# Performance work log

Hardware: AMD Instinct MI355X
Metric: run time of the kernel (lower is better)

## Reference

```python
import jax, jax.numpy as jnp
import numpy as np

NUM_GROUPS = 32
EPS = 1e-5


def group_norm(x, w, b):
    # x: [B,C,H,W], 32 groups
    B, C, H, W = x.shape
    xg = x.reshape(B, NUM_GROUPS, C // NUM_GROUPS, H, W)
    mean = xg.mean(axis=(2, 3, 4), keepdims=True)
    var = xg.var(axis=(2, 3, 4), keepdims=True)
    xn = ((xg - mean) * jax.lax.rsqrt(var + EPS)).reshape(B, C, H, W)
    return xn * w[None, :, None, None] + b[None, :, None, None]


def conv1x1(x, w, b):
    # x: [B,C,H,W], w: [O,C], b: [O]
    return jnp.einsum('bchw,oc->bohw', x, w) + b[None, :, None, None]


def setup_inputs() -> dict:
    key = jax.random.key(0)
    ks = jax.random.split(key, 7)
    B, C, H, W = 16, 512, 32, 32
    x = jax.random.normal(ks[0], (B, C, H, W), dtype=jnp.float32)
    gn_w = jnp.ones((C,), dtype=jnp.float32)
    gn_b = jnp.zeros((C,), dtype=jnp.float32)
    s = 1.0 / np.sqrt(C)
    qkv_w = jax.random.normal(ks[1], (3 * C, C), dtype=jnp.float32) * s
    qkv_b = jnp.zeros((3 * C,), dtype=jnp.float32)
    proj_w = jax.random.normal(ks[2], (C, C), dtype=jnp.float32) * s
    proj_b = jnp.zeros((C,), dtype=jnp.float32)
    return {"x": x, "gn_w": gn_w, "gn_b": gn_b, "qkv_w": qkv_w,
            "qkv_b": qkv_b, "proj_w": proj_w, "proj_b": proj_b}


def reference(x, gn_w, gn_b, qkv_w, qkv_b, proj_w, proj_b):
    B, C, H, W = x.shape
    qkv = conv1x1(group_norm(x, gn_w, gn_b), qkv_w, qkv_b)
    q, k, v = jnp.split(qkv, 3, axis=1)
    scale = (C // 8) ** (-0.5)
    # attn: [B, h, w, H, W]
    attn = jnp.einsum('bchw,bcHW->bhwHW', q * scale, k)
    # NOTE: faithful to original torch code: softmax over the LAST axis only
    attn = jax.nn.softmax(attn, axis=-1)
    out = jnp.einsum('bhwHW,bcHW->bchw', attn, v)
    return x + conv1x1(out, proj_w, proj_b)
```

## Files before the change

kernel.cpp:

```cpp
#include <hip/hip_runtime.h>
#include <hip/hip_bf16.h>

#define B_    16
#define C_    512
#define S_    1024
#define NGRP  32
#define CPG   16

typedef __attribute__((ext_vector_type(8))) short  short8;
typedef __attribute__((ext_vector_type(4))) short  short4v;
typedef __attribute__((ext_vector_type(4))) float  floatx4;

__device__ __forceinline__ unsigned short f2bf(float f) {
    __hip_bfloat16 h = __float2bfloat16(f);
    unsigned short u;
    __builtin_memcpy(&u, &h, 2);
    return u;
}

__global__ __launch_bounds__(256)
void gn_fused_kernel(const float* __restrict__ x, const float* __restrict__ w,
                     const float* __restrict__ bias, __hip_bfloat16* __restrict__ xnT) {
    int bg = blockIdx.x;
    int b = bg >> 5, g = bg & 31;
    const float4* xp = (const float4*)(x + (size_t)bg * (CPG * S_));
    int tid = threadIdx.x;

    float4 vv[16];
    float s = 0.f, ss = 0.f;
#pragma unroll
    for (int r = 0; r < 16; ++r) {
        float4 v = xp[r * 256 + tid];
        vv[r] = v;
        s  += v.x + v.y + v.z + v.w;
        ss += v.x*v.x + v.y*v.y + v.z*v.z + v.w*v.w;
    }
    for (int off = 32; off > 0; off >>= 1) {
        s  += __shfl_down(s, off);
        ss += __shfl_down(ss, off);
    }
    __shared__ float red[2][4];
    __shared__ float msh[2];
    int wid = tid >> 6, lane = tid & 63;
    if (lane == 0) { red[0][wid] = s; red[1][wid] = ss; }
    __syncthreads();
    if (tid == 0) {
        float a = 0.f, c = 0.f;
        for (int i = 0; i < 4; ++i) { a += red[0][i]; c += red[1][i]; }
        float mean = a / (float)(CPG * S_);
        float var  = c / (float)(CPG * S_) - mean * mean;
        msh[0] = mean;
        msh[1] = rsqrtf(var + 1e-5f);
    }
    __syncthreads();
    float mean = msh[0], inv = msh[1];

    float sc[16], sh[16];
#pragma unroll
    for (int c = 0; c < 16; ++c) {
        float wc = w[g * 16 + c];
        sc[c] = inv * wc;
        sh[c] = bias[g * 16 + c] - mean * inv * wc;
    }

#pragma unroll
    for (int kk = 0; kk < 4; ++kk) {
        unsigned short outp[16];
#pragma unroll
        for (int c = 0; c < 16; ++c) {
            float v = (kk == 0) ? vv[c].x : (kk == 1) ? vv[c].y : (kk == 2) ? vv[c].z : vv[c].w;
            outp[c] = f2bf(v * sc[c] + sh[c]);
        }
        int srow = 4 * tid + kk;
        unsigned short* dst = (unsigned short*)xnT + ((size_t)(b * S_ + srow) * C_ + g * 16);
        *(short8*)dst       = *(short8*)outp;
        *(short8*)(dst + 8) = *(short8*)(outp + 8);
    }
}

__global__ __launch_bounds__(256)
void prep_kernel(const float* __restrict__ qkv_w, const float* __restrict__ proj_w,
                 const float* __restrict__ qkv_b,
                 unsigned short* __restrict__ bufX,
                 unsigned short* __restrict__ bufY,
                 float* __restrict__ bqWk, float* __restrict__ biasvp)
{
    int blk = blockIdx.x;
    int tid = threadIdx.x;
    if (blk < 192) {
        __shared__ float T[64][65];
        int mat = blk >> 6, tile = blk & 63;
        int r0 = (tile >> 3) * 64, c0 = (tile & 7) * 64;
        const float* src; unsigned short* dst;
        if (mat == 0)      { src = qkv_w + 512 * 512;  dst = bufX; }
        else if (mat == 1) { src = qkv_w;              dst = bufY; }
        else               { src = qkv_w + 1024 * 512; dst = bufY + 262144; }
#pragma unroll
        for (int rr = 0; rr < 4; ++rr) {
            int sr = rr * 16 + (tid >> 4);
            int sc = (tid & 15) * 4;
            float4 v = *(const float4*)(src + (size_t)(c0 + sr) * 512 + r0 + sc);
            T[sc][sr] = v.x; T[sc + 1][sr] = v.y; T[sc + 2][sr] = v.z; T[sc + 3][sr] = v.w;
        }
        __syncthreads();
#pragma unroll
        for (int rr = 0; rr < 4; ++rr) {
            int dr = rr * 16 + (tid >> 4);
            int dc = (tid & 15) * 4;
            short4v o;
            o[0] = (short)f2bf(T[dr][dc]);     o[1] = (short)f2bf(T[dr][dc + 1]);
            o[2] = (short)f2bf(T[dr][dc + 2]); o[3] = (short)f2bf(T[dr][dc + 3]);
            *(short4v*)(dst + (size_t)(r0 + dr) * 512 + c0 + dc) = o;
        }
    } else if (blk < 256) {
        unsigned short* wp = bufX + 262144;
#pragma unroll
        for (int t = 0; t < 4; ++t) {
            int i = (blk - 192) * 4096 + t * 1024 + tid * 4;
            float4 v = *(const float4*)(proj_w + i);
            short4v o;
            o[0] = (short)f2bf(v.x); o[1] = (short)f2bf(v.y);
            o[2] = (short)f2bf(v.z); o[3] = (short)f2bf(v.w);
            *(short4v*)(wp + i) = o;
        }
    } else if (blk < 264) {
        int sub = blk - 256;
        int j = (sub & 1) * 256 + tid;
        int o0 = (sub >> 1) * 128;
        float acc = 0.f;
#pragma unroll 8
        for (int oo = 0; oo < 128; ++oo) {
            int o = o0 + oo;
            acc += qkv_b[o] * qkv_w[(size_t)(512 + o) * 512 + j];
        }
        atomicAdd(&bqWk[j], acc);
    } else {
        int wv = tid >> 6, lane = tid & 63;
        int c = (blk - 264) * 4 + wv;
        float s = 0.f;
#pragma unroll
        for (int t = 0; t < 8; ++t)
            s += proj_w[(size_t)c * 512 + t * 64 + lane] * qkv_b[1024 + t * 64 + lane];
        for (int off = 32; off > 0; off >>= 1) s += __shfl_down(s, off);
        if (lane == 0) biasvp[c] = s;
    }
}

template<int BIAS_MODE, bool OUT_BF16, bool RESID, bool SWIZ, int KTOT>
__global__ __launch_bounds__(256)
void mfma_gemm(const unsigned short* __restrict__ A, const unsigned short* __restrict__ Bm,
               const float* __restrict__ bias, const float* __restrict__ resid,
               void* __restrict__ Yv,
               int lda, int ldb, int ldy,
               size_t sA, size_t sB, size_t sY, size_t sR, float alpha,
               int ntsh, int nxsh)
{
    __shared__ unsigned short As[2 * 128 * 32];
    __shared__ unsigned short Bs[2 * 128 * 32];
    int bx, by, bz;
    if (SWIZ) {
        int lin = blockIdx.x;
        int xcd = lin & 7, sup = lin >> 3;
        bz = xcd + ((sup >> ntsh) << 3);
        int tile = sup & ((1 << ntsh) - 1);
        bx = tile & ((1 << nxsh) - 1);
        by = tile >> nxsh;
    } else { bx = blockIdx.x; by = blockIdx.y; bz = blockIdx.z; }

    const unsigned short* Ab = A  + (size_t)bz * sA;
    const unsigned short* Bb = Bm + (size_t)bz * sB;
    const int tid = threadIdx.x, wave = tid >> 6, lane = tid & 63;
    const int m0 = by * 128, n0 = bx * 128;
    const int wr = wave >> 1, wc = wave & 1, lr = lane & 15, kq = lane >> 4;
    const int row0 = tid >> 2, kc0 = (tid & 3) << 3;

    floatx4 acc[4][4] = {};

    for (int k0 = 0; k0 < KTOT; k0 += 64) {
        __syncthreads();
#pragma unroll
        for (int kk = 0; kk < 2; ++kk) {
#pragma unroll
            for (int r = 0; r < 2; ++r) {
                const unsigned short* ga = Ab + (size_t)(m0 + r * 64 + row0) * lda + k0 + kk * 32 + kc0;
                __builtin_amdgcn_global_load_lds(
                    (const __attribute__((address_space(1))) void*)ga,
                    (__attribute__((address_space(3))) void*)(As + kk * 4096 + (r * 256 + wave * 64) * 8),
                    16, 0, 0);
                const unsigned short* gb = Bb + (size_t)(n0 + r * 64 + row0) * ldb + k0 + kk * 32 + kc0;
                __builtin_amdgcn_global_load_lds(
                    (const __attribute__((address_space(1))) void*)gb,
                    (__attribute__((address_space(3))) void*)(Bs + kk * 4096 + (r * 256 + wave * 64) * 8),
                    16, 0, 0);
            }
        }
        __syncthreads();

#pragma unroll
        for (int kk = 0; kk < 2; ++kk) {
            short8 af[4], bfr[4];
#pragma unroll
            for (int i = 0; i < 4; ++i)
                af[i] = *(const short8*)&As[kk * 4096 + (wr * 64 + i * 16 + lr) * 32 + kq * 8];
#pragma unroll
            for (int j = 0; j < 4; ++j)
                bfr[j] = *(const short8*)&Bs[kk * 4096 + (wc * 64 + j * 16 + lr) * 32 + kq * 8];
#pragma unroll
            for (int i = 0; i < 4; ++i)
#pragma unroll
                for (int j = 0; j < 4; ++j)
                    acc[i][j] = __builtin_amdgcn_mfma_f32_16x16x32_bf16(af[i], bfr[j], acc[i][j], 0, 0, 0);
        }
    }

    const size_t ybase = (size_t)bz * sY;
    const size_t rbase = (size_t)bz * sR;
#pragma unroll
    for (int i = 0; i < 4; ++i) {
#pragma unroll
        for (int r = 0; r < 4; ++r) {
            int m = m0 + wr * 64 + i * 16 + kq * 4 + r;
            float bm = (BIAS_MODE == 1) ? bias[m] : 0.f;
#pragma unroll
            for (int j = 0; j < 4; ++j) {
                int n = n0 + wc * 64 + j * 16 + lr;
                float vv = acc[i][j][r] * alpha + bm;
                if (BIAS_MODE == 2) vv += bias[n];
                if (RESID) vv += resid[rbase + (size_t)m * ldy + n];
                if (OUT_BF16)
                    ((__hip_bfloat16*)Yv)[ybase + (size_t)m * ldy + n] = __float2bfloat16(vv);
                else
                    ((float*)Yv)[ybase + (size_t)m * ldy + n] = vv;
            }
        }
    }
}

template<int BIAS_MODE, bool OUT_BF16, bool RESID, bool SWIZ, int KTOT>
__global__ __launch_bounds__(512)
void gemm8ph(const unsigned short* __restrict__ A, const unsigned short* __restrict__ Bm,
             const float* __restrict__ bias, const float* __restrict__ resid,
             void* __restrict__ Yv,
             int lda, int ldb, int ldy,
             size_t sA, size_t sB, size_t sY, size_t sR, float alpha,
             int ntsh, int nxsh)
{
    __shared__ __align__(16) char lds[98304];
    char* asb = lds;
    char* bsb = lds + 32768;

    int bx, by, bz;
    if (SWIZ) {
        int lin = blockIdx.x;
        int xcd = lin & 7, sup = lin >> 3;
        bz = xcd + ((sup >> ntsh) << 3);
        int tile = sup & ((1 << ntsh) - 1);
        bx = tile & ((1 << nxsh) - 1);
        by = tile >> nxsh;
    } else { bx = blockIdx.x; by = blockIdx.y; bz = blockIdx.z; }

    const unsigned short* Ab = A  + (size_t)bz * sA;
    const unsigned short* Bb = Bm + (size_t)bz * sB;
    const int tid = threadIdx.x, wave = tid >> 6, lane = tid & 63;
    const int m0 = by * 128, n0 = bx * 256;
    const int wr = wave >> 2, wc = wave & 3;
    const int lr = lane & 15, kq = lane >> 4;
    const int swz = (lr & 7) << 4;

    floatx4 acc[4][4] = {};
    short8 aF[2][2], bF[2][2][2];

    auto stage = [&](const unsigned short* __restrict__ G, int ld, int grow,
                     int t, char* dstbase) {
#pragma unroll
        for (int c = 0; c < 2; ++c) {
            int x = c * 8192 + tid * 16;
            int row = x >> 7;
            int colb = (x & 127) ^ ((row & 7) << 4);
            const unsigned short* ga = G + (size_t)(grow + row) * ld + t * 64 + (colb >> 1);
            char* ldst = dstbase + c * 8192 + wave * 1024;
            __builtin_amdgcn_global_load_lds(
                (const __attribute__((address_space(1))) void*)ga,
                (__attribute__((address_space(3))) void*)ldst, 16, 0, 0);
        }
    };
    auto rdA = [&](int buf, int i, int kk) {
        int byte = buf * 16384 + (wr * 64 + i * 16 + lr) * 128
                 + ((kk * 64 + kq * 16) ^ swz);
        return *(const short8*)(asb + byte);
    };
    auto rdB = [&](int buf, int jn, int kk) {
        int row = wc * 64 + jn * 16 + lr;
        int byte = buf * 32768 + (row >> 7) * 16384 + (row & 127) * 128
                 + ((kk * 64 + kq * 16) ^ swz);
        return *(const short8*)(bsb + byte);
    };

    stage(Ab, lda, m0,       0, asb);
    stage(Bb, ldb, n0,       0, bsb);
    stage(Bb, ldb, n0 + 128, 0, bsb + 16384);
    stage(Bb, ldb, n0,       1, bsb + 32768);
    stage(Bb, ldb, n0 + 128, 1, bsb + 32768 + 16384);
    asm volatile("s_waitcnt vmcnt(4)" ::: "memory");
    __builtin_amdgcn_s_barrier();

    constexpr int NT = KTOT / 64;
    for (int t = 0; t < NT; ++t) {
        const int buf = t & 1;
#pragma unroll
        for (int ii = 0; ii < 2; ++ii) { aF[ii][0] = rdA(buf, ii, 0); aF[ii][1] = rdA(buf, ii, 1); }
#pragma unroll
        for (int jj = 0; jj < 2; ++jj) { bF[0][jj][0] = rdB(buf, jj, 0); bF[0][jj][1] = rdB(buf, jj, 1); }
        if (t < NT - 1) stage(Ab, lda, m0, t + 1, asb + ((t + 1) & 1) * 16384);
        __builtin_amdgcn_s_barrier();
        asm volatile("s_waitcnt lgkmcnt(0)" ::: "memory");
        __builtin_amdgcn_s_setprio(1);
#pragma unroll
        for (int ii = 0; ii < 2; ++ii)
#pragma unroll
            for (int jj = 0; jj < 2; ++jj)
#pragma unroll
                for (int kk = 0; kk < 2; ++kk)
                    acc[ii][jj] = __builtin_amdgcn_mfma_f32_16x16x32_bf16(aF[ii][kk], bF[0][jj][kk], acc[ii][jj], 0, 0, 0);
        __builtin_amdgcn_s_setprio(0);
        __builtin_amdgcn_s_barrier();
#pragma unroll
        for (int jj = 0; jj < 2; ++jj) { bF[1][jj][0] = rdB(buf, 2 + jj, 0); bF[1][jj][1] = rdB(buf, 2 + jj, 1); }
        __builtin_amdgcn_s_barrier();
        asm volatile("s_waitcnt lgkmcnt(0)" ::: "memory");
        __builtin_amdgcn_s_setprio(1);
#pragma unroll
        for (int ii = 0; ii < 2; ++ii)
#pragma unroll
            for (int jj = 0; jj < 2; ++jj)
#pragma unroll
                for (int kk = 0; kk < 2; ++kk)
                    acc[ii][2 + jj] = __builtin_amdgcn_mfma_f32_16x16x32_bf16(aF[ii][kk], bF[1][jj][kk], acc[ii][2 + jj], 0, 0, 0);
        __builtin_amdgcn_s_setprio(0);
        __builtin_amdgcn_s_barrier();
#pragma unroll
        for (int ii = 0; ii < 2; ++ii) { aF[ii][0] = rdA(buf, 2 + ii, 0); aF[ii][1] = rdA(buf, 2 + ii, 1); }
        if (t < NT - 2) stage(Bb, ldb, n0, t + 2, bsb + buf * 32768);
        __builtin_amdgcn_s_barrier();
        asm volatile("s_waitcnt lgkmcnt(0)" ::: "memory");
        __builtin_amdgcn_s_setprio(1);
#pragma unroll
        for (int ii = 0; ii < 2; ++ii)
#pragma unroll
            for (int jj = 0; jj < 2; ++jj)
#pragma unroll
                for (int kk = 0; kk < 2; ++kk)
                    acc[2 + ii][2 + jj] = __builtin_amdgcn_mfma_f32_16x16x32_bf16(aF[ii][kk], bF[1][jj][kk], acc[2 + ii][2 + jj], 0, 0, 0);
        __builtin_amdgcn_s_setprio(0);
        __builtin_amdgcn_s_barrier();
        if (t < NT - 2) stage(Bb, ldb, n0 + 128, t + 2, bsb + buf * 32768 + 16384);
        __builtin_amdgcn_s_setprio(1);
#pragma unroll
        for (int ii = 0; ii < 2; ++ii)
#pragma unroll
            for (int jj = 0; jj < 2; ++jj)
#pragma unroll
                for (int kk = 0; kk < 2; ++kk)
                    acc[2 + ii][jj] = __builtin_amdgcn_mfma_f32_16x16x32_bf16(aF[ii][kk], bF[0][jj][kk], acc[2 + ii][jj], 0, 0, 0);
        __builtin_amdgcn_s_setprio(0);
        if (t < NT - 2) { asm volatile("s_waitcnt vmcnt(4)" ::: "memory"); }
        else            { asm volatile("s_waitcnt vmcnt(0)" ::: "memory"); }
        __builtin_amdgcn_s_barrier();
    }

    const size_t ybase = (size_t)bz * sY;
    const size_t rbase = (size_t)bz * sR;
#pragma unroll
    for (int i = 0; i < 4; ++i) {
#pragma unroll
        for (int r = 0; r < 4; ++r) {
            int m = m0 + wr * 64 + i * 16 + kq * 4 + r;
            float bm = (BIAS_MODE == 1) ? bias[m] : 0.f;
#pragma unroll
            for (int j = 0; j < 4; ++j) {
                int n = n0 + wc * 64 + j * 16 + lr;
                float vv = acc[i][j][r] * alpha + bm;
                if (BIAS_MODE == 2) vv += bias[n];
                if (RESID) vv += resid[rbase + (size_t)m * ldy + n];
                if (OUT_BF16)
                    ((__hip_bfloat16*)Yv)[ybase + (size_t)m * ldy + n] = __float2bfloat16(vv);
                else
                    ((float*)Yv)[ybase + (size_t)m * ldy + n] = vv;
            }
        }
    }
}

__global__ __launch_bounds__(512)
void scores_softmax8(const unsigned short* __restrict__ A,
                     const unsigned short* __restrict__ Bm,
                     unsigned short* __restrict__ P)
{
    __shared__ __align__(16) unsigned short lds[65536];
    char* asb = (char*)lds;
    char* bsb = (char*)lds + 65536;

    const int bid = blockIdx.x;
    const int bz = bid >> 4, t16 = bid & 15;
    const int by = t16 >> 2, bx = t16 & 3;
    const int m0 = by << 8, n0 = bx << 8;

    const size_t sAB = (size_t)S_ * 512;
    const unsigned short* Ab = A  + (size_t)bz * sAB;
    const unsigned short* Bb = Bm + (size_t)bz * sAB;

    const int tid = threadIdx.x, wave = tid >> 6, lane = tid & 63;
    const int wr = wave >> 2, wc = wave & 3;
    const int lr = lane & 15, kq = lane >> 4;
    const int swz = (lr & 7) << 4;

    floatx4 acc[8][4] = {};
    short8 aF[4][2], bF[2][2][2];

    auto stage = [&](const unsigned short* __restrict__ G, int row0, int t,
                     char* base, int buf, int half) {
#pragma unroll
        for (int c = 0; c < 2; ++c) {
            int x = c * 8192 + tid * 16;
            int row = x >> 7;
            int colb = (x & 127) ^ ((row & 7) << 4);
            const unsigned short* ga = G + (((size_t)(row0 + row)) << 9) + (t << 6) + (colb >> 1);
            char* ldst = base + buf * 32768 + half * 16384 + c * 8192 + wave * 1024;
            __builtin_amdgcn_global_load_lds(
                (const __attribute__((address_space(1))) void*)ga,
                (__attribute__((address_space(3))) void*)ldst, 16, 0, 0);
        }
    };
    auto rdA = [&](int buf, int mh, int ii, int kk) {
        int byte = buf * 32768 + wr * 16384 + (mh * 64 + ii * 16 + lr) * 128
                 + ((kk * 64 + kq * 16) ^ swz);
        return *(const short8*)(asb + byte);
    };
    auto rdB = [&](int buf, int nh, int jj, int kk) {
        int trow = wc * 64 + (nh * 2 + jj) * 16 + lr;
        int byte = buf * 32768 + (trow >> 7) * 16384 + (trow & 127) * 128
                 + ((kk * 64 + kq * 16) ^ swz);
        return *(const short8*)(bsb + byte);
    };

    stage(Ab, m0,       0, asb, 0, 0);
    stage(Bb, n0,       0, bsb, 0, 0);
    stage(Bb, n0 + 128, 0, bsb, 0, 1);
    stage(Ab, m0 + 128, 0, asb, 0, 1);
    stage(Ab, m0,       1, asb, 1, 0);
    stage(Bb, n0,       1, bsb, 1, 0);
    stage(Bb, n0 + 128, 1, bsb, 1, 1);
    asm volatile("s_waitcnt vmcnt(6)" ::: "memory");
    __builtin_amdgcn_s_barrier();

    for (int t = 0; t < 8; ++t) {
        const int buf = t & 1;
#pragma unroll
        for (int ii = 0; ii < 4; ++ii) { aF[ii][0] = rdA(buf, 0, ii, 0); aF[ii][1] = rdA(buf, 0, ii, 1); }
#pragma unroll
        for (int jj = 0; jj < 2; ++jj) { bF[0][jj][0] = rdB(buf, 0, jj, 0); bF[0][jj][1] = rdB(buf, 0, jj, 1); }
        if (t < 7) stage(Ab, m0 + 128, t + 1, asb, (t + 1) & 1, 1);
        __builtin_amdgcn_s_barrier();
        asm volatile("s_waitcnt lgkmcnt(0)" ::: "memory");
        __builtin_amdgcn_s_setprio(1);
#pragma unroll
        for (int ii = 0; ii < 4; ++ii)
#pragma unroll
            for (int jj = 0; jj < 2; ++jj)
#pragma unroll
                for (int kk = 0; kk < 2; ++kk)
                    acc[ii][jj] = __builtin_amdgcn_mfma_f32_16x16x32_bf16(aF[ii][kk], bF[0][jj][kk], acc[ii][jj], 0, 0, 0);
        __builtin_amdgcn_s_setprio(0);
        __builtin_amdgcn_s_barrier();
#pragma unroll
        for (int jj = 0; jj < 2; ++jj) { bF[1][jj][0] = rdB(buf, 1, jj, 0); bF[1][jj][1] = rdB(buf, 1, jj, 1); }
        __builtin_amdgcn_s_barrier();
        asm volatile("s_waitcnt lgkmcnt(0)" ::: "memory");
        __builtin_amdgcn_s_setprio(1);
#pragma unroll
        for (int ii = 0; ii < 4; ++ii)
#pragma unroll
            for (int jj = 0; jj < 2; ++jj)
#pragma unroll
                for (int kk = 0; kk < 2; ++kk)
                    acc[ii][2 + jj] = __builtin_amdgcn_mfma_f32_16x16x32_bf16(aF[ii][kk], bF[1][jj][kk], acc[ii][2 + jj], 0, 0, 0);
        __builtin_amdgcn_s_setprio(0);
        __builtin_amdgcn_s_barrier();
#pragma unroll
        for (int ii = 0; ii < 4; ++ii) { aF[ii][0] = rdA(buf, 1, ii, 0); aF[ii][1] = rdA(buf, 1, ii, 1); }
        if (t < 6) stage(Bb, n0, t + 2, bsb, buf, 0);
        __builtin_amdgcn_s_barrier();
        asm volatile("s_waitcnt lgkmcnt(0)" ::: "memory");
        __builtin_amdgcn_s_setprio(1);
#pragma unroll
        for (int ii = 0; ii < 4; ++ii)
#pragma unroll
            for (int jj = 0; jj < 2; ++jj)
#pragma unroll
                for (int kk = 0; kk < 2; ++kk)
                    acc[4 + ii][2 + jj] = __builtin_amdgcn_mfma_f32_16x16x32_bf16(aF[ii][kk], bF[1][jj][kk], acc[4 + ii][2 + jj], 0, 0, 0);
        __builtin_amdgcn_s_setprio(0);
        __builtin_amdgcn_s_barrier();
        if (t < 6) {
            stage(Ab, m0,       t + 2, asb, buf, 0);
            stage(Bb, n0 + 128, t + 2, bsb, buf, 1);
        }
        __builtin_amdgcn_s_setprio(1);
#pragma unroll
        for (int ii = 0; ii < 4; ++ii)
#pragma unroll
            for (int jj = 0; jj < 2; ++jj)
#pragma unroll
                for (int kk = 0; kk < 2; ++kk)
                    acc[4 + ii][jj] = __builtin_amdgcn_mfma_f32_16x16x32_bf16(aF[ii][kk], bF[0][jj][kk], acc[4 + ii][jj], 0, 0, 0);
        __builtin_amdgcn_s_setprio(0);
        if (t < 6) { asm volatile("s_waitcnt vmcnt(6)" ::: "memory"); }
        else       { asm volatile("s_waitcnt vmcnt(0)" ::: "memory"); }
        __builtin_amdgcn_s_barrier();
    }

#pragma unroll
    for (int j = 0; j < 4; ++j) {
        int sqc = wc * 64 + j * 16 + lr;
        int srow = sqc * 512;
        int sxor = (sqc & 7) << 4;
#pragma unroll
        for (int h = 0; h < 4; ++h) {
            float v0[4], v1[4];
            float mx = -1e30f;
#pragma unroll
            for (int r = 0; r < 4; ++r) {
                v0[r] = acc[2 * h][j][r]     * 0.125f;
                v1[r] = acc[2 * h + 1][j][r] * 0.125f;
                mx = fmaxf(mx, fmaxf(v0[r], v1[r]));
            }
            mx = fmaxf(mx, __shfl_xor(mx, 16));
            mx = fmaxf(mx, __shfl_xor(mx, 32));
            float sm = 0.f;
#pragma unroll
            for (int r = 0; r < 4; ++r) {
                v0[r] = __expf(v0[r] - mx);
                v1[r] = __expf(v1[r] - mx);
                sm += v0[r] + v1[r];
            }
            sm += __shfl_xor(sm, 16);
            sm += __shfl_xor(sm, 32);
            float inv = 1.f / sm;
            short4v p0, p1;
#pragma unroll
            for (int r = 0; r < 4; ++r) {
                p0[r] = (short)f2bf(v0[r] * inv);
                p1[r] = (short)f2bf(v1[r] * inv);
            }
            int kb = (wr * 128 + h * 32 + kq * 4) * 2;
            *(short4v*)(asb + ((srow + kb) ^ sxor))      = p0;
            *(short4v*)(asb + ((srow + kb + 32) ^ sxor)) = p1;
        }
    }
    __syncthreads();

    const size_t pbase = ((size_t)bz << 20) + (size_t)n0 * 1024 + m0;
#pragma unroll
    for (int it = 0; it < 16; ++it) {
        int row = wave * 32 + it * 2 + (lane >> 5);
        int colb = (lane & 31) << 4;
        short8 v = *(const short8*)(asb + ((row * 512 + colb) ^ ((row & 7) << 4)));
        *(short8*)(P + pbase + (size_t)row * 1024 + (colb >> 1)) = v;
    }
}

extern "C" void kernel_launch(void* const* d_in, const int* in_sizes, int n_in,
                              void* d_out, int out_size, void* d_ws, size_t ws_size,
                              hipStream_t stream) {
    const float* x     = (const float*)d_in[0];
    const float* gn_w  = (const float*)d_in[1];
    const float* gn_b  = (const float*)d_in[2];
    const float* qkv_w = (const float*)d_in[3];
    const float* qkv_b = (const float*)d_in[4];
    const float* pr_w  = (const float*)d_in[5];
    const float* pr_b  = (const float*)d_in[6];
    float* out = (float*)d_out;

    char* w = (char*)d_ws;
    __hip_bfloat16* xnT  = (__hip_bfloat16*)w;
    __hip_bfloat16* u    = (__hip_bfloat16*)(w + (16u << 20));
    __hip_bfloat16* Vp   = (__hip_bfloat16*)(w + (32u << 20));
    __hip_bfloat16* P    = (__hip_bfloat16*)(w + (48u << 20));
    unsigned short* bufX = (unsigned short*)(w + (80u << 20));
    unsigned short* bufY = (unsigned short*)(w + (81u << 20));
    unsigned short* bufZ = (unsigned short*)(w + (82u << 20));
    float*          bqWk = (float*)(w + (83u << 20));
    float*          bvp  = (float*)(w + (83u << 20) + 4096);

    hipMemsetAsync(bqWk, 0, 512 * sizeof(float), stream);

    prep_kernel<<<392, 256, 0, stream>>>(qkv_w, pr_w, qkv_b, bufX, bufY, bqWk, bvp);

    gn_fused_kernel<<<B_ * NGRP, 256, 0, stream>>>(x, gn_w, gn_b, xnT);

    mfma_gemm<0, true, false, false, 512><<<dim3(4, 4, 2), 256, 0, stream>>>(
        bufX, bufY, nullptr, nullptr, bufZ,
        512, 512, 512, 262144, 262144, 262144, 0, 1.f, 0, 0);

    gemm8ph<2, true, false, false, 512><<<dim3(2, 128, 1), 512, 0, stream>>>(
        (const unsigned short*)xnT, bufZ, bqWk, nullptr, u,
        512, 512, 512, 0, 0, 0, 0, 1.f, 0, 0);

    gemm8ph<1, true, false, true, 512><<<256, 512, 0, stream>>>(
        bufZ + 262144, (const unsigned short*)xnT, bvp, nullptr, Vp,
        512, 512, 1024, 0, (size_t)S_ * 512, (size_t)512 * S_, 0, 1.f, 4, 2);

    scores_softmax8<<<256, 512, 0, stream>>>(
        (const unsigned short*)xnT, (const unsigned short*)u, (unsigned short*)P);

    gemm8ph<1, false, true, true, 1024><<<256, 512, 0, stream>>>(
        (const unsigned short*)Vp, (const unsigned short*)P, pr_b, x, out,
        1024, 1024, 1024, (size_t)512 * S_, (size_t)S_ * S_, (size_t)512 * S_,
        (size_t)512 * S_, 1.f, 4, 2);
}
```

Measured before the change: 197.8 us.

## Merge group-norm with weight-product GEMM and fuse the two projection GEMMs

Group-norm and the small weight-product GEMM (bufX×bufY→bufZ) now run in one launch, with blocks split by index: the first 512 do normalization and the last 32 do the GEMM. The two independent projection GEMMs (u and Vp) also share one 512-block launch through a common device body. This removes two kernel launches and the idle tail between small dependent kernels. The cost is a merged kernel whose resource use is set by the heavier branch, which may lower occupancy for the group-norm blocks.

```diff
diff --git a/kernel.cpp b/kernel.cpp
--- a/kernel.cpp
+++ b/kernel.cpp
@@ -16,66 +16,6 @@
     unsigned short u;
     __builtin_memcpy(&u, &h, 2);
     return u;
-}
-
-__global__ __launch_bounds__(256)
-void gn_fused_kernel(const float* __restrict__ x, const float* __restrict__ w,
-                     const float* __restrict__ bias, __hip_bfloat16* __restrict__ xnT) {
-    int bg = blockIdx.x;
-    int b = bg >> 5, g = bg & 31;
-    const float4* xp = (const float4*)(x + (size_t)bg * (CPG * S_));
-    int tid = threadIdx.x;
-
-    float4 vv[16];
-    float s = 0.f, ss = 0.f;
-#pragma unroll
-    for (int r = 0; r < 16; ++r) {
-        float4 v = xp[r * 256 + tid];
-        vv[r] = v;
-        s  += v.x + v.y + v.z + v.w;
-        ss += v.x*v.x + v.y*v.y + v.z*v.z + v.w*v.w;
-    }
-    for (int off = 32; off > 0; off >>= 1) {
-        s  += __shfl_down(s, off);
-        ss += __shfl_down(ss, off);
-    }
-    __shared__ float red[2][4];
-    __shared__ float msh[2];
-    int wid = tid >> 6, lane = tid & 63;
-    if (lane == 0) { red[0][wid] = s; red[1][wid] = ss; }
-    __syncthreads();
-    if (tid == 0) {
-        float a = 0.f, c = 0.f;
-        for (int i = 0; i < 4; ++i) { a += red[0][i]; c += red[1][i]; }
-        float mean = a / (float)(CPG * S_);
-        float var  = c / (float)(CPG * S_) - mean * mean;
-        msh[0] = mean;
-        msh[1] = rsqrtf(var + 1e-5f);
-    }
-    __syncthreads();
-    float mean = msh[0], inv = msh[1];
-
-    float sc[16], sh[16];
-#pragma unroll
-    for (int c = 0; c < 16; ++c) {
-        float wc = w[g * 16 + c];
-        sc[c] = inv * wc;
-        sh[c] = bias[g * 16 + c] - mean * inv * wc;
-    }
-
-#pragma unroll
-    for (int kk = 0; kk < 4; ++kk) {
-        unsigned short outp[16];
-#pragma unroll
-        for (int c = 0; c < 16; ++c) {
-            float v = (kk == 0) ? vv[c].x : (kk == 1) ? vv[c].y : (kk == 2) ? vv[c].z : vv[c].w;
-            outp[c] = f2bf(v * sc[c] + sh[c]);
-        }
-        int srow = 4 * tid + kk;
-        unsigned short* dst = (unsigned short*)xnT + ((size_t)(b * S_ + srow) * C_ + g * 16);
-        *(short8*)dst       = *(short8*)outp;
-        *(short8*)(dst + 8) = *(short8*)(outp + 8);
-    }
 }
 
 __global__ __launch_bounds__(256)
@@ -146,77 +86,250 @@
     }
 }
 
-template<int BIAS_MODE, bool OUT_BF16, bool RESID, bool SWIZ, int KTOT>
 __global__ __launch_bounds__(256)
-void mfma_gemm(const unsigned short* __restrict__ A, const unsigned short* __restrict__ Bm,
-               const float* __restrict__ bias, const float* __restrict__ resid,
-               void* __restrict__ Yv,
-               int lda, int ldb, int ldy,
-               size_t sA, size_t sB, size_t sY, size_t sR, float alpha,
-               int ntsh, int nxsh)
+void gn_plus_w(const float* __restrict__ x, const float* __restrict__ gnw,
+               const float* __restrict__ gnb, __hip_bfloat16* __restrict__ xnT,
+               const unsigned short* __restrict__ bufX,
+               const unsigned short* __restrict__ bufY,
+               unsigned short* __restrict__ bufZ)
 {
-    __shared__ unsigned short As[2 * 128 * 32];
-    __shared__ unsigned short Bs[2 * 128 * 32];
-    int bx, by, bz;
-    if (SWIZ) {
-        int lin = blockIdx.x;
-        int xcd = lin & 7, sup = lin >> 3;
-        bz = xcd + ((sup >> ntsh) << 3);
-        int tile = sup & ((1 << ntsh) - 1);
-        bx = tile & ((1 << nxsh) - 1);
-        by = tile >> nxsh;
-    } else { bx = blockIdx.x; by = blockIdx.y; bz = blockIdx.z; }
-
-    const unsigned short* Ab = A  + (size_t)bz * sA;
-    const unsigned short* Bb = Bm + (size_t)bz * sB;
+    __shared__ __align__(16) char smem[32832];
+    int blk = blockIdx.x;
+    int tid = threadIdx.x;
+
+    if (blk < 512) {
+        int b = blk >> 5, g = blk & 31;
+        const float4* xp = (const float4*)(x + (size_t)blk * (CPG * S_));
+        float4 vv[16];
+        float s = 0.f, ss = 0.f;
+#pragma unroll
+        for (int r = 0; r < 16; ++r) {
+            float4 v = xp[r * 256 + tid];
+            vv[r] = v;
+            s  += v.x + v.y + v.z + v.w;
+            ss += v.x*v.x + v.y*v.y + v.z*v.z + v.w*v.w;
+        }
+        for (int off = 32; off > 0; off >>= 1) {
+            s  += __shfl_down(s, off);
+            ss += __shfl_down(ss, off);
+        }
+        float* red = (float*)(smem + 32768);
+        float* msh = (float*)(smem + 32800);
+        int wid = tid >> 6, lane = tid & 63;
+        if (lane == 0) { red[wid] = s; red[4 + wid] = ss; }
+        __syncthreads();
+        if (tid == 0) {
+            float a = 0.f, c = 0.f;
+            for (int i = 0; i < 4; ++i) { a += red[i]; c += red[4 + i]; }
+            float mean = a / (float)(CPG * S_);
+            float var  = c / (float)(CPG * S_) - mean * mean;
+            msh[0] = mean;
+            msh[1] = rsqrtf(var + 1e-5f);
+        }
+        __syncthreads();
+        float mean = msh[0], inv = msh[1];
+
+        float sc[16], sh[16];
+#pragma unroll
+        for (int c = 0; c < 16; ++c) {
+            float wc = gnw[g * 16 + c];
+            sc[c] = inv * wc;
+            sh[c] = gnb[g * 16 + c] - mean * inv * wc;
+        }
+#pragma unroll
+        for (int kk = 0; kk < 4; ++kk) {
+            unsigned short outp[16];
+#pragma unroll
+            for (int c = 0; c < 16; ++c) {
+                float v = (kk == 0) ? vv[c].x : (kk == 1) ? vv[c].y : (kk == 2) ? vv[c].z : vv[c].w;
+                outp[c] = f2bf(v * sc[c] + sh[c]);
+            }
+            int srow = 4 * tid + kk;
+            unsigned short* dst = (unsigned short*)xnT + ((size_t)(b * S_ + srow) * C_ + g * 16);
+            *(short8*)dst       = *(short8*)outp;
+            *(short8*)(dst + 8) = *(short8*)(outp + 8);
+        }
+    } else {
+        unsigned short* As = (unsigned short*)smem;
+        unsigned short* Bs = (unsigned short*)(smem + 16384);
+        int id = blk - 512;
+        int bx = id & 3, by = (id >> 2) & 3, bz = id >> 4;
+        const unsigned short* Ab = bufX + (size_t)bz * 262144;
+        const unsigned short* Bb = bufY + (size_t)bz * 262144;
+        __hip_bfloat16* Y = (__hip_bfloat16*)bufZ + (size_t)bz * 262144;
+        const int wave = tid >> 6, lane = tid & 63;
+        const int m0 = by * 128, n0 = bx * 128;
+        const int wr = wave >> 1, wc = wave & 1, lr = lane & 15, kq = lane >> 4;
+        const int row0 = tid >> 2, kc0 = (tid & 3) << 3;
+
+        floatx4 acc[4][4] = {};
+        for (int k0 = 0; k0 < 512; k0 += 64) {
+            __syncthreads();
+#pragma unroll
+            for (int kk = 0; kk < 2; ++kk) {
+#pragma unroll
+                for (int r = 0; r < 2; ++r) {
+                    const unsigned short* ga = Ab + (size_t)(m0 + r * 64 + row0) * 512 + k0 + kk * 32 + kc0;
+                    __builtin_amdgcn_global_load_lds(
+                        (const __attribute__((address_space(1))) void*)ga,
+                        (__attribute__((address_space(3))) void*)(As + kk * 4096 + (r * 256 + wave * 64) * 8),
+                        16, 0, 0);
+                    const unsigned short* gb = Bb + (size_t)(n0 + r * 64 + row0) * 512 + k0 + kk * 32 + kc0;
+                    __builtin_amdgcn_global_load_lds(
+                        (const __attribute__((address_space(1))) void*)gb,
+                        (__attribute__((address_space(3))) void*)(Bs + kk * 4096 + (r * 256 + wave * 64) * 8),
+                        16, 0, 0);
+                }
+            }
+            __syncthreads();
+#pragma unroll
+            for (int kk = 0; kk < 2; ++kk) {
+                short8 af[4], bfr[4];
+#pragma unroll
+                for (int i = 0; i < 4; ++i)
+                    af[i] = *(const short8*)&As[kk * 4096 + (wr * 64 + i * 16 + lr) * 32 + kq * 8];
+#pragma unroll
+                for (int j = 0; j < 4; ++j)
+                    bfr[j] = *(const short8*)&Bs[kk * 4096 + (wc * 64 + j * 16 + lr) * 32 + kq * 8];
+#pragma unroll
+                for (int i = 0; i < 4; ++i)
+#pragma unroll
+                    for (int j = 0; j < 4; ++j)
+                        acc[i][j] = __builtin_amdgcn_mfma_f32_16x16x32_bf16(af[i], bfr[j], acc[i][j], 0, 0, 0);
+            }
+        }
+#pragma unroll
+        for (int i = 0; i < 4; ++i)
+#pragma unroll
+            for (int r = 0; r < 4; ++r) {
+                int m = m0 + wr * 64 + i * 16 + kq * 4 + r;
+#pragma unroll
+                for (int j = 0; j < 4; ++j) {
+                    int n = n0 + wc * 64 + j * 16 + lr;
+                    Y[(size_t)m * 512 + n] = __float2bfloat16(acc[i][j][r]);
+                }
+            }
+    }
+}
+
+template<int BIAS_MODE>
+__device__ __forceinline__
+void gemm8_body(char* lds, const unsigned short* __restrict__ Ab,
+                const unsigned short* __restrict__ Bb,
+                const float* __restrict__ bias,
+                __hip_bfloat16* __restrict__ Y,
+                int lda, int ldb, int ldy, size_t ybase, int m0, int n0)
+{
+    char* asb = lds;
+    char* bsb = lds + 32768;
     const int tid = threadIdx.x, wave = tid >> 6, lane = tid & 63;
-    const int m0 = by * 128, n0 = bx * 128;
-    const int wr = wave >> 1, wc = wave & 1, lr = lane & 15, kq = lane >> 4;
-    const int row0 = tid >> 2, kc0 = (tid & 3) << 3;
+    const int wr = wave >> 2, wc = wave & 3;
+    const int lr = lane & 15, kq = lane >> 4;
+    const int swz = (lr & 7) << 4;
 
     floatx4 acc[4][4] = {};
-
-    for (int k0 = 0; k0 < KTOT; k0 += 64) {
-        __syncthreads();
-#pragma unroll
-        for (int kk = 0; kk < 2; ++kk) {
-#pragma unroll
-            for (int r = 0; r < 2; ++r) {
-                const unsigned short* ga = Ab + (size_t)(m0 + r * 64 + row0) * lda + k0 + kk * 32 + kc0;
-                __builtin_amdgcn_global_load_lds(
-                    (const __attribute__((address_space(1))) void*)ga,
-                    (__attribute__((address_space(3))) void*)(As + kk * 4096 + (r * 256 + wave * 64) * 8),
-                    16, 0, 0);
-                const unsigned short* gb = Bb + (size_t)(n0 + r * 64 + row0) * ldb + k0 + kk * 32 + kc0;
-                __builtin_amdgcn_global_load_lds(
-                    (const __attribute__((address_space(1))) void*)gb,
-                    (__attribute__((address_space(3))) void*)(Bs + kk * 4096 + (r * 256 + wave * 64) * 8),
-                    16, 0, 0);
-            }
-        }
-        __syncthreads();
-
-#pragma unroll
-        for (int kk = 0; kk < 2; ++kk) {
-            short8 af[4], bfr[4];
-#pragma unroll
-            for (int i = 0; i < 4; ++i)
-                af[i] = *(const short8*)&As[kk * 4096 + (wr * 64 + i * 16 + lr) * 32 + kq * 8];
-#pragma unroll
-            for (int j = 0; j < 4; ++j)
-                bfr[j] = *(const short8*)&Bs[kk * 4096 + (wc * 64 + j * 16 + lr) * 32 + kq * 8];
-#pragma unroll
-            for (int i = 0; i < 4; ++i)
-#pragma unroll
-                for (int j = 0; j < 4; ++j)
-                    acc[i][j] = __builtin_amdgcn_mfma_f32_16x16x32_bf16(af[i], bfr[j], acc[i][j], 0, 0, 0);
-        }
-    }
-
-    const size_t ybase = (size_t)bz * sY;
-    const size_t rbase = (size_t)bz * sR;
-#pragma unroll
-    for (int i = 0; i < 4; ++i) {
+    short8 aF[2][2], bF[2][2][2];
+
+    auto stage = [&](const unsigned short* __restrict__ G, int ld, int grow,
+                     int t, char* dstbase) {
+#pragma unroll
+        for (int c = 0; c < 2; ++c) {
+            int x = c * 8192 + tid * 16;
+            int row = x >> 7;
+            int colb = (x & 127) ^ ((row & 7) << 4);
+            const unsigned short* ga = G + (size_t)(grow + row) * ld + t * 64 + (colb >> 1);
+            char* ldst = dstbase + c * 8192 + wave * 1024;
+            __builtin_amdgcn_global_load_lds(
+                (const __attribute__((address_space(1))) void*)ga,
+                (__attribute__((address_space(3))) void*)ldst, 16, 0, 0);
+        }
+    };
+    auto rdA = [&](int buf, int i, int kk) {
+        int byte = buf * 16384 + (wr * 64 + i * 16 + lr) * 128
+                 + ((kk * 64 + kq * 16) ^ swz);
+        return *(const short8*)(asb + byte);
+    };
+    auto rdB = [&](int buf, int jn, int kk) {
+        int row = wc * 64 + jn * 16 + lr;
+        int byte = buf * 32768 + (row >> 7) * 16384 + (row & 127) * 128
+                 + ((kk * 64 + kq * 16) ^ swz);
+        return *(const short8*)(bsb + byte);
+    };
+
+    stage(Ab, lda, m0,       0, asb);
+    stage(Bb, ldb, n0,       0, bsb);
+    stage(Bb, ldb, n0 + 128, 0, bsb + 16384);
+    stage(Bb, ldb, n0,       1, bsb + 32768);
+    stage(Bb, ldb, n0 + 128, 1, bsb + 32768 + 16384);
+    asm volatile("s_waitcnt vmcnt(4)" ::: "memory");
+    __builtin_amdgcn_s_barrier();
+
+    constexpr int NT = 8;
+    for (int t = 0; t < NT; ++t) {
+        const int buf = t & 1;
+#pragma unroll
+        for (int ii = 0; ii < 2; ++ii) { aF[ii][0] = rdA(buf, ii, 0); aF[ii][1] = rdA(buf, ii, 1); }
+#pragma unroll
+        for (int jj = 0; jj < 2; ++jj) { bF[0][jj][0] = rdB(buf, jj, 0); bF[0][jj][1] = rdB(buf, jj, 1); }
+        if (t < NT - 1) stage(Ab, lda, m0, t + 1, asb + ((t + 1) & 1) * 16384);
+        __builtin_amdgcn_s_barrier();
+        asm volatile("s_waitcnt lgkmcnt(0)" ::: "memory");
+        __builtin_amdgcn_s_setprio(1);
+#pragma unroll
+        for (int ii = 0; ii < 2; ++ii)
+#pragma unroll
+            for (int jj = 0; jj < 2; ++jj)
+#pragma unroll
+                for (int kk = 0; kk < 2; ++kk)
+                    acc[ii][jj] = __builtin_amdgcn_mfma_f32_16x16x32_bf16(aF[ii][kk], bF[0][jj][kk], acc[ii][jj], 0, 0, 0);
+        __builtin_amdgcn_s_setprio(0);
+        __builtin_amdgcn_s_barrier();
+#pragma unroll
+        for (int jj = 0; jj < 2; ++jj) { bF[1][jj][0] = rdB(buf, 2 + jj, 0); bF[1][jj][1] = rdB(buf, 2 + jj, 1); }
+        __builtin_amdgcn_s_barrier();
+        asm volatile("s_waitcnt lgkmcnt(0)" ::: "memory");
+        __builtin_amdgcn_s_setprio(1);
+#pragma unroll
+        for (int ii = 0; ii < 2; ++ii)
+#pragma unroll
+            for (int jj = 0; jj < 2; ++jj)
+#pragma unroll
+                for (int kk = 0; kk < 2; ++kk)
+                    acc[ii][2 + jj] = __builtin_amdgcn_mfma_f32_16x16x32_bf16(aF[ii][kk], bF[1][jj][kk], acc[ii][2 + jj], 0, 0, 0);
+        __builtin_amdgcn_s_setprio(0);
+        __builtin_amdgcn_s_barrier();
+#pragma unroll
+        for (int ii = 0; ii < 2; ++ii) { aF[ii][0] = rdA(buf, 2 + ii, 0); aF[ii][1] = rdA(buf, 2 + ii, 1); }
+        if (t < NT - 2) stage(Bb, ldb, n0, t + 2, bsb + buf * 32768);
+        __builtin_amdgcn_s_barrier();
+        asm volatile("s_waitcnt lgkmcnt(0)" ::: "memory");
+        __builtin_amdgcn_s_setprio(1);
+#pragma unroll
+        for (int ii = 0; ii < 2; ++ii)
+#pragma unroll
+            for (int jj = 0; jj < 2; ++jj)
+#pragma unroll
+                for (int kk = 0; kk < 2; ++kk)
+                    acc[2 + ii][2 + jj] = __builtin_amdgcn_mfma_f32_16x16x32_bf16(aF[ii][kk], bF[1][jj][kk], acc[2 + ii][2 + jj], 0, 0, 0);
+        __builtin_amdgcn_s_setprio(0);
+        __builtin_amdgcn_s_barrier();
+        if (t < NT - 2) stage(Bb, ldb, n0 + 128, t + 2, bsb + buf * 32768 + 16384);
+        __builtin_amdgcn_s_setprio(1);
+#pragma unroll
+        for (int ii = 0; ii < 2; ++ii)
+#pragma unroll
+            for (int jj = 0; jj < 2; ++jj)
+#pragma unroll
+                for (int kk = 0; kk < 2; ++kk)
+                    acc[2 + ii][jj] = __builtin_amdgcn_mfma_f32_16x16x32_bf16(aF[ii][kk], bF[0][jj][kk], acc[2 + ii][jj], 0, 0, 0);
+        __builtin_amdgcn_s_setprio(0);
+        if (t < NT - 2) { asm volatile("s_waitcnt vmcnt(4)" ::: "memory"); }
+        else            { asm volatile("s_waitcnt vmcnt(0)" ::: "memory"); }
+        __builtin_amdgcn_s_barrier();
+    }
+
+#pragma unroll
+    for (int i = 0; i < 4; ++i)
 #pragma unroll
         for (int r = 0; r < 4; ++r) {
             int m = m0 + wr * 64 + i * 16 + kq * 4 + r;
@@ -224,15 +337,34 @@
 #pragma unroll
             for (int j = 0; j < 4; ++j) {
                 int n = n0 + wc * 64 + j * 16 + lr;
-                float vv = acc[i][j][r] * alpha + bm;
+                float vv = acc[i][j][r] + bm;
                 if (BIAS_MODE == 2) vv += bias[n];
-                if (RESID) vv += resid[rbase + (size_t)m * ldy + n];
-                if (OUT_BF16)
-                    ((__hip_bfloat16*)Yv)[ybase + (size_t)m * ldy + n] = __float2bfloat16(vv);
-                else
-                    ((float*)Yv)[ybase + (size_t)m * ldy + n] = vv;
-            }
-        }
+                Y[ybase + (size_t)m * ldy + n] = __float2bfloat16(vv);
+            }
+        }
+}
+
+__global__ __launch_bounds__(512)
+void fused_s45(const unsigned short* __restrict__ xnT,
+               const unsigned short* __restrict__ bufZ,
+               const float* __restrict__ bqWk, const float* __restrict__ bvp,
+               __hip_bfloat16* __restrict__ u, __hip_bfloat16* __restrict__ Vp)
+{
+    __shared__ __align__(16) char lds[98304];
+    int blk = blockIdx.x;
+    if (blk < 256) {
+        int by = blk >> 1, bx = blk & 1;
+        gemm8_body<2>(lds, xnT, bufZ, bqWk, u,
+                      512, 512, 512, 0, by * 128, bx * 256);
+    } else {
+        int lin = blk - 256;
+        int xcd = lin & 7, sup = lin >> 3;
+        int bz = xcd + ((sup >> 4) << 3);
+        int tile = sup & 15;
+        int bx = tile & 3, by = tile >> 2;
+        gemm8_body<1>(lds, bufZ + 262144, xnT + (size_t)bz * ((size_t)S_ * 512),
+                      bvp, Vp,
+                      512, 512, 1024, (size_t)bz * 512 * S_, by * 128, bx * 256);
     }
 }
 
@@ -596,19 +728,10 @@
 
     prep_kernel<<<392, 256, 0, stream>>>(qkv_w, pr_w, qkv_b, bufX, bufY, bqWk, bvp);
 
-    gn_fused_kernel<<<B_ * NGRP, 256, 0, stream>>>(x, gn_w, gn_b, xnT);
-
-    mfma_gemm<0, true, false, false, 512><<<dim3(4, 4, 2), 256, 0, stream>>>(
-        bufX, bufY, nullptr, nullptr, bufZ,
-        512, 512, 512, 262144, 262144, 262144, 0, 1.f, 0, 0);
-
-    gemm8ph<2, true, false, false, 512><<<dim3(2, 128, 1), 512, 0, stream>>>(
-        (const unsigned short*)xnT, bufZ, bqWk, nullptr, u,
-        512, 512, 512, 0, 0, 0, 0, 1.f, 0, 0);
-
-    gemm8ph<1, true, false, true, 512><<<256, 512, 0, stream>>>(
-        bufZ + 262144, (const unsigned short*)xnT, bvp, nullptr, Vp,
-        512, 512, 1024, 0, (size_t)S_ * 512, (size_t)512 * S_, 0, 1.f, 4, 2);
+    gn_plus_w<<<544, 256, 0, stream>>>(x, gn_w, gn_b, xnT, bufX, bufY, bufZ);
+
+    fused_s45<<<512, 512, 0, stream>>>((const unsigned short*)xnT, bufZ, bqWk, bvp,
+                                       u, Vp);
 
     scores_softmax8<<<256, 512, 0, stream>>>(
         (const unsigned short*)xnT, (const unsigned short*)u, (unsigned short*)P);
```

Measured after the change: 196.4 us. Within noise of the previous version (-0.7%).
